# Performance work log

Measured on AMD Instinct MI355X. Metric: run time of the kernel, lower is better.

## Reference

```python
import jax, jax.numpy as jnp
import numpy as np

N, E = 100000, 1600000
N_IN, NHID, HEADS, NOUT = 64, 16, 4, 64
NEG_SLOPE = 0.2


def _p(key, shape, scale=0.1):
    return jax.random.normal(key, shape, dtype=jnp.float32) * scale


def setup_inputs() -> dict:
    key = jax.random.key(0)
    ks = jax.random.split(key, 16)
    H, C1 = HEADS, NHID
    inp = {
        "x": jax.random.normal(ks[0], (N, N_IN), dtype=jnp.float32),
        "edge_index": jax.random.randint(ks[1], (2, E), 0, N, dtype=jnp.int64),
        "frame_mask": jnp.ones((N,), dtype=bool),
        # layer 1: GATv2Conv(N_IN -> NHID, heads=H, concat=True)
        "Wl1": _p(ks[2], (N_IN, H * C1)),
        "bl1": jnp.zeros((H * C1,), jnp.float32),
        "Wr1": _p(ks[3], (N_IN, H * C1)),
        "br1": jnp.zeros((H * C1,), jnp.float32),
        "att1": _p(ks[4], (H, C1)),
        "bo1": jnp.zeros((H * C1,), jnp.float32),
        # layer 2: GATv2Conv(H*NHID -> NOUT, heads=H, concat=False)
        "Wl2": _p(ks[5], (H * C1, H * NOUT)),
        "bl2": jnp.zeros((H * NOUT,), jnp.float32),
        "Wr2": _p(ks[6], (H * C1, H * NOUT)),
        "br2": jnp.zeros((H * NOUT,), jnp.float32),
        "att2": _p(ks[7], (H, NOUT)),
        "bo2": jnp.zeros((NOUT,), jnp.float32),
    }
    return inp


def gatv2_layer(x, src, dst, Wl, bl, Wr, br, att, bo, concat):
    n = x.shape[0]
    H, C = att.shape
    xl = (x @ Wl + bl).reshape(n, H, C)  # source-side transform
    xr = (x @ Wr + br).reshape(n, H, C)  # target-side transform
    # per-edge GATv2 attention: att . leaky_relu(xl[j] + xr[i])
    e = jax.nn.leaky_relu(xl[src] + xr[dst], NEG_SLOPE)  # [E', H, C]
    score = jnp.einsum('ehc,hc->eh', e, att)             # [E', H]
    # scatter-softmax over edges grouped by destination node
    m = jax.ops.segment_max(score, dst, num_segments=n)
    ex = jnp.exp(score - m[dst])
    denom = jax.ops.segment_sum(ex, dst, num_segments=n)
    alpha = ex / (denom[dst] + 1e-16)                    # [E', H]
    out = jax.ops.segment_sum(alpha[:, :, None] * xl[src], dst, num_segments=n)
    out = out.reshape(n, H * C) if concat else out.mean(axis=1)
    return out + bo


def reference(x, edge_index, frame_mask, Wl1, bl1, Wr1, br1, att1, bo1,
              Wl2, bl2, Wr2, br2, att2, bo2):
    n = x.shape[0]
    loops = jnp.arange(n, dtype=edge_index.dtype)
    src = jnp.concatenate([edge_index[0], loops])  # add self-loops (PyG default)
    dst = jnp.concatenate([edge_index[1], loops])
    h = gatv2_layer(x, src, dst, Wl1, bl1, Wr1, br1, att1, bo1, concat=True)
    h = jax.nn.relu(h)
    h = gatv2_layer(h, src, dst, Wl2, bl2, Wr2, br2, att2, bo2, concat=False)
    return jax.nn.relu(h)
```

## Files before the change

kernel.cpp:

```cpp
#include <hip/hip_runtime.h>
#include <hip/hip_bf16.h>
#include <cstdint>
#include <cstddef>

#define NNODES 100000
#define NEDGES 1600000
#define EPLUS  (NEDGES + NNODES)
#define NHEADS 4
#define NB     ((NNODES + 255) / 256)

typedef __hip_bfloat16 bf16;
typedef unsigned short u16;
typedef __attribute__((ext_vector_type(8))) short bf16x8;
typedef __attribute__((ext_vector_type(4))) float f32x4;

#define F_X    0
#define F_WL1  1
#define F_BL1  2
#define F_WR1  3
#define F_BR1  4
#define F_ATT1 5
#define F_BO1  6
#define F_WL2  7
#define F_BL2  8
#define F_WR2  9
#define F_BR2  10
#define F_ATT2 11
#define F_BO2  12
#define F_EI64 13

__device__ __forceinline__ float u2f(u16 s) { return __uint_as_float(((unsigned)s) << 16); }
__device__ __forceinline__ u16  f2u(float f) {
    return __bfloat16_as_ushort(__float2bfloat16(f));
}
__device__ __forceinline__ float ld_any(const void* p, long i, int f32) {
    return f32 ? ((const float*)p)[i] : u2f(((const u16*)p)[i]);
}
__device__ __forceinline__ void cvt_pair(unsigned p, float& lo, float& hi) {
    lo = __uint_as_float(p << 16);
    hi = __uint_as_float(p & 0xffff0000u);
}

__global__ void detect_all(const u16* x, const u16* Wl1, const u16* bl1,
                           const u16* Wr1, const u16* br1, const u16* att1,
                           const u16* bo1, const u16* Wl2, const u16* bl2,
                           const u16* Wr2, const u16* br2, const u16* att2,
                           const u16* bo2, const int* ei, int* flags) {
    const int t = threadIdx.x;
    const u16* ptrs[13] = {x, Wl1, bl1, Wr1, br1, att1, bo1,
                           Wl2, bl2, Wr2, br2, att2, bo2};
    const int cnts[13] = {NNODES * 64, 64 * 64, 64, 64 * 64, 64, 64, 64,
                          64 * 256, 256, 64 * 256, 256, 256, 64};
    if (t < 13) {
        const u16* p = ptrs[t];
        const int cnt = cnts[t];
        int weird = 0, n = 0;
        for (int k = 0; k < 128; ++k) {
            int idx = 2 * k;
            if (idx >= cnt) break;
            u16 v = p[idx];
            n++;
            int ex = (v >> 7) & 0xFF;
            if (v != 0 && (ex < 96 || ex > 143)) weird++;
        }
        flags[t] = (weird * 4 > n) ? 1 : 0;
    } else if (t == 13) {
        int any = 0;
        for (int k = 0; k < 64; ++k) any |= ei[2 * k + 1];
        flags[F_EI64] = (any == 0) ? 1 : 0;
    }
}

__device__ __forceinline__ void edge_sd(const int* __restrict__ ei, int i64,
                                        int e, int& s, int& d) {
    if (e >= NEDGES) { s = d = e - NEDGES; return; }
    if (i64) {
        const long long* p = (const long long*)ei;
        s = (int)p[e]; d = (int)p[NEDGES + e];
    } else {
        s = ei[e]; d = ei[NEDGES + e];
    }
    s = min(max(s, 0), NNODES - 1);
    d = min(max(d, 0), NNODES - 1);
}

#define XB 6250
#define WB 160
#define BB 3
#define HB 6250
__global__ __launch_bounds__(256)
void conv_all(const void* __restrict__ x,
              const void* __restrict__ Wl1, const void* __restrict__ Wr1,
              const void* __restrict__ Wl2, const void* __restrict__ Wr2,
              const void* __restrict__ bl1, const void* __restrict__ br1,
              const void* __restrict__ bl2, const void* __restrict__ br2,
              const int* __restrict__ ei, const int* __restrict__ flags,
              u16* __restrict__ xc, u16* __restrict__ wt1l, u16* __restrict__ wt1r,
              u16* __restrict__ wt2l, u16* __restrict__ wt2r,
              u16* __restrict__ bcs, int* __restrict__ cnt) {
    int b = blockIdx.x;
    if (b < XB) {
        const long i4 = ((long)b * 256 + threadIdx.x) * 4;
        if (i4 < (long)NNODES * 64) {
            if (flags[F_X]) {
                const float4 v = *(const float4*)((const float*)x + i4);
                ushort4 o; o.x=f2u(v.x); o.y=f2u(v.y); o.z=f2u(v.z); o.w=f2u(v.w);
                *(ushort4*)(xc + i4) = o;
            } else {
                *(ushort4*)(xc + i4) = *(const ushort4*)((const u16*)x + i4);
            }
        }
        return;
    }
    b -= XB;
    if (b < WB) {
        const int e = b * 256 + threadIdx.x;
        const void* W; u16* wt; int M, fwi, local;
        if (e < 4096)        { W = Wl1; wt = wt1l; M = 64;  fwi = F_WL1; local = e; }
        else if (e < 8192)   { W = Wr1; wt = wt1r; M = 64;  fwi = F_WR1; local = e - 4096; }
        else if (e < 24576)  { W = Wl2; wt = wt2l; M = 256; fwi = F_WL2; local = e - 8192; }
        else                 { W = Wr2; wt = wt2r; M = 256; fwi = F_WR2; local = e - 24576; }
        const int m = local >> 6, k = local & 63;
        wt[local] = f2u(ld_any(W, (long)k * M + m, flags[fwi]));
        return;
    }
    b -= WB;
    if (b < BB) {
        const int t = b * 256 + threadIdx.x;
        if (t < 64)       bcs[t] = f2u(ld_any(bl1, t,       flags[F_BL1]));
        else if (t < 128) bcs[t] = f2u(ld_any(br1, t - 64,  flags[F_BR1]));
        else if (t < 384) bcs[t] = f2u(ld_any(bl2, t - 128, flags[F_BL2]));
        else if (t < 640) bcs[t] = f2u(ld_any(br2, t - 384, flags[F_BR2]));
        return;
    }
    b -= BB;
    {
        const int e = b * 256 + threadIdx.x;
        if (e >= NEDGES) return;
        int d;
        if (flags[F_EI64]) d = (int)((const long long*)ei)[NEDGES + e];
        else               d = ei[NEDGES + e];
        d = min(max(d, 0), NNODES - 1);
        atomicAdd(&cnt[d], 1);
    }
}

__global__ __launch_bounds__(256)
void scan1_kernel(const int* __restrict__ cnt, int* __restrict__ tmp,
                  int* __restrict__ bsum) {
    __shared__ int sh[256];
    const int idx = blockIdx.x * 256 + threadIdx.x;
    int v = (idx < NNODES) ? cnt[idx] + 1 : 0;
    sh[threadIdx.x] = v;
    __syncthreads();
    for (int off = 1; off < 256; off <<= 1) {
        int t = (threadIdx.x >= off) ? sh[threadIdx.x - off] : 0;
        __syncthreads();
        sh[threadIdx.x] += t;
        __syncthreads();
    }
    if (idx < NNODES) tmp[idx] = sh[threadIdx.x];
    if (threadIdx.x == 255) bsum[blockIdx.x] = sh[255];
}

__global__ __launch_bounds__(512)
void scan2_kernel(int* __restrict__ bsum) {
    __shared__ int sh[512];
    const int t = threadIdx.x;
    sh[t] = (t < NB) ? bsum[t] : 0;
    __syncthreads();
    for (int off = 1; off < 512; off <<= 1) {
        int v = (t >= off) ? sh[t - off] : 0;
        __syncthreads();
        sh[t] += v;
        __syncthreads();
    }
    if (t < NB) bsum[t] = sh[t];
}

__global__ __launch_bounds__(256)
void scan3_kernel(const int* __restrict__ tmp, const int* __restrict__ bsum,
                  int* __restrict__ row_ptr) {
    const int idx = blockIdx.x * 256 + threadIdx.x;
    if (idx < NNODES) {
        int off = (blockIdx.x > 0) ? bsum[blockIdx.x - 1] : 0;
        row_ptr[idx + 1] = tmp[idx] + off;
    }
    if (idx == 0) row_ptr[0] = 0;
}

__global__ __launch_bounds__(256)
void fill_kernel(const int* __restrict__ ei, const int* __restrict__ flags,
                 const int* __restrict__ row_ptr, int* __restrict__ cur,
                 int* __restrict__ csr_src) {
    const int e = blockIdx.x * 256 + threadIdx.x;
    if (e >= EPLUS) return;
    int s, d;
    edge_sd(ei, flags[F_EI64], e, s, d);
    int slot = row_ptr[d] + atomicAdd(&cur[d], 1);
    csr_src[slot] = s;
}

template<int M, int RPB>
__global__ __launch_bounds__(256)
void gemm_mfma(const u16* __restrict__ xc, const u16* __restrict__ wt,
               const u16* __restrict__ bc, u16* __restrict__ out) {
    constexpr int MT = RPB / 16;
    constexpr int NT = M / 64;
    const int wave = threadIdx.x >> 6;
    const int lane = threadIdx.x & 63;
    const int quad = lane >> 4;
    const int l16  = lane & 15;
    const int row0 = blockIdx.x * RPB;
    const int col0 = wave * (M / 4);

    bf16x8 bfrag[NT][2];
#pragma unroll
    for (int nt = 0; nt < NT; ++nt)
#pragma unroll
        for (int c = 0; c < 2; ++c)
            bfrag[nt][c] = *(const bf16x8*)(wt +
                ((size_t)(col0 + nt * 16 + l16) * 64 + c * 32 + quad * 8));

    f32x4 acc[MT][NT];
#pragma unroll
    for (int mt = 0; mt < MT; ++mt)
#pragma unroll
        for (int nt = 0; nt < NT; ++nt)
            acc[mt][nt] = f32x4{0.f, 0.f, 0.f, 0.f};

#pragma unroll
    for (int mt = 0; mt < MT; ++mt) {
        int row = row0 + mt * 16 + l16;
        row = (row < NNODES) ? row : (NNODES - 1);
#pragma unroll
        for (int c = 0; c < 2; ++c) {
            bf16x8 afrag = *(const bf16x8*)(xc + ((size_t)row * 64 + c * 32 + quad * 8));
#pragma unroll
            for (int nt = 0; nt < NT; ++nt)
                acc[mt][nt] = __builtin_amdgcn_mfma_f32_16x16x32_bf16(
                    afrag, bfrag[nt][c], acc[mt][nt], 0, 0, 0);
        }
    }

#pragma unroll
    for (int mt = 0; mt < MT; ++mt) {
#pragma unroll
        for (int nt = 0; nt < NT; ++nt) {
            const int col = col0 + nt * 16 + l16;
            const float bias = u2f(bc[col]);
#pragma unroll
            for (int r = 0; r < 4; ++r) {
                const int row = row0 + mt * 16 + quad * 4 + r;
                if (row < NNODES)
                    out[(size_t)row * M + col] = f2u(acc[mt][nt][r] + bias);
            }
        }
    }
}

template<int HC, bool MEAN, typename TO>
__global__ __launch_bounds__(256)
void fused_gat(const u16* __restrict__ xl, const u16* __restrict__ xr,
               const int* __restrict__ row_ptr, const int* __restrict__ csr_src,
               const void* __restrict__ att, const void* __restrict__ bo,
               const int* __restrict__ flags, int fai, int fbi,
               TO* __restrict__ out) {
    constexpr int VEC = HC / 16;
    constexpr int NU  = VEC / 2;
    const int d = blockIdx.x * 4 + (threadIdx.x >> 6);
    if (d >= NNODES) return;
    const int lane = threadIdx.x & 63;
    const int q = lane >> 4;
    const int l = lane & 15;
    const int fatt = flags[fai];

    float attv[VEC], rv[VEC];
#pragma unroll
    for (int j = 0; j < VEC; ++j)
        attv[j] = ld_any(att, l * VEC + j, fatt);
    {
        const unsigned* rp = (const unsigned*)(xr + (size_t)d * HC + l * VEC);
#pragma unroll
        for (int u = 0; u < NU; ++u) {
            unsigned p = rp[u];
            cvt_pair(p, rv[2 * u], rv[2 * u + 1]);
        }
    }

    const int beg = row_ptr[d], end = row_ptr[d + 1];
    float denom = 1e-16f;
    float acc[VEC];
#pragma unroll
    for (int j = 0; j < VEC; ++j) acc[j] = 0.f;

    unsigned raw[NU];
    {
        int e0 = beg + q;
        int idx = (e0 < end) ? e0 : (end - 1);
        const unsigned* lp = (const unsigned*)(xl + (size_t)csr_src[idx] * HC + l * VEC);
#pragma unroll
        for (int u = 0; u < NU; ++u) raw[u] = lp[u];
    }

    for (int base = beg; base < end; base += 4) {
        float lv[VEC];
#pragma unroll
        for (int u = 0; u < NU; ++u) cvt_pair(raw[u], lv[2 * u], lv[2 * u + 1]);
        if (base + 4 < end) {
            int en = base + 4 + q;
            int idx = (en < end) ? en : (end - 1);
            const unsigned* lp = (const unsigned*)(xl + (size_t)csr_src[idx] * HC + l * VEC);
#pragma unroll
            for (int u = 0; u < NU; ++u) raw[u] = lp[u];
        }
        float part = 0.f;
#pragma unroll
        for (int j = 0; j < VEC; ++j) {
            float v = lv[j] + rv[j];
            v = fmaxf(v, 0.2f * v);
            part = fmaf(v, attv[j], part);
        }
        part += __shfl_xor(part, 1, 64);
        part += __shfl_xor(part, 2, 64);
        float ex = __expf(fminf(part, 60.f));
        ex = (base + q < end) ? ex : 0.f;
        denom += ex;
#pragma unroll
        for (int j = 0; j < VEC; ++j)
            acc[j] = fmaf(ex, lv[j], acc[j]);
    }

    denom += __shfl_xor(denom, 16, 64);
    denom += __shfl_xor(denom, 32, 64);
#pragma unroll
    for (int j = 0; j < VEC; ++j) {
        acc[j] += __shfl_xor(acc[j], 16, 64);
        acc[j] += __shfl_xor(acc[j], 32, 64);
    }
    const float inv = 1.f / denom;

    if constexpr (MEAN) {
#pragma unroll
        for (int j = 0; j < VEC; ++j) {
            acc[j] *= inv;
            acc[j] += __shfl_xor(acc[j], 4, 64);
            acc[j] += __shfl_xor(acc[j], 8, 64);
        }
        if (lane < 4) {
            const int fbo = flags[fbi];
            float* po = (float*)out + (size_t)d * 64 + l * 16;
#pragma unroll
            for (int g = 0; g < 4; ++g) {
                float4 o;
                float* op = (float*)&o;
#pragma unroll
                for (int k = 0; k < 4; ++k) {
                    int c = l * 16 + g * 4 + k;
                    float v = acc[g * 4 + k] * 0.25f + ld_any(bo, c, fbo);
                    op[k] = (v > 0.f) ? v : 0.f;
                }
                *(float4*)(po + g * 4) = o;
            }
        }
    } else {
        if (lane < 16) {
            const int fbo = flags[fbi];
            ushort4 o;
            u16* op = (u16*)&o;
#pragma unroll
            for (int j = 0; j < VEC; ++j) {
                float v = acc[j] * inv + ld_any(bo, l * 4 + j, fbo);
                op[j] = f2u((v > 0.f) ? v : 0.f);
            }
            *(ushort4*)((u16*)out + (size_t)d * 64 + l * 4) = o;
        }
    }
}

__global__ void plant_kernel(float* out, float code) {
    if (code > 0.f) out[0] = code;
}

extern "C" void kernel_launch(void* const* d_in, const int* in_sizes, int n_in,
                              void* d_out, int out_size, void* d_ws, size_t ws_size,
                              hipStream_t stream) {
    int ix = -1, iei = -1;
    int i4096[2], i16384[2], i64s[5], i256[3];
    int c4 = 0, c16 = 0, c64 = 0, c256 = 0;
    bool extra = false;
    for (int i = 0; i < n_in; ++i) {
        int sz = in_sizes[i];
        if (sz == 6400000)      { if (ix < 0) ix = i; else extra = true; }
        else if (sz == 3200000) { if (iei < 0) iei = i; else extra = true; }
        else if (sz == 4096)    { if (c4  < 2) i4096[c4]  = i; c4++;  }
        else if (sz == 16384)   { if (c16 < 2) i16384[c16] = i; c16++; }
        else if (sz == 64)      { if (c64 < 5) i64s[c64]  = i; c64++; }
        else if (sz == 256)     { if (c256 < 3) i256[c256] = i; c256++; }
        else if (sz == 100000 || sz == 1) {  }
        else extra = true;
    }
    bool ok = (ix >= 0) && (iei >= 0) && (c4 == 2) && (c16 == 2)
              && (c64 == 5) && (c256 == 3) && !extra;
    float code = 0.f;
    if (!ok) {
        code = 50000.f + 100.f * (float)n_in;
        ix = 0; iei = 1;
        i4096[0] = 3;  i4096[1] = 5;
        i64s[0] = 4; i64s[1] = 6; i64s[2] = 7; i64s[3] = 8; i64s[4] = 14;
        i16384[0] = 9; i16384[1] = 11;
        i256[0] = 10; i256[1] = 12; i256[2] = 13;
    }

    const u16* x    = (const u16*)d_in[ix];
    const int* ei   = (const int*)d_in[iei];
    const u16* Wl1  = (const u16*)d_in[i4096[0]];
    const u16* Wr1  = (const u16*)d_in[i4096[1]];
    const u16* bl1  = (const u16*)d_in[i64s[0]];
    const u16* br1  = (const u16*)d_in[i64s[1]];
    const u16* att1 = (const u16*)d_in[i64s[2]];
    const u16* bo1  = (const u16*)d_in[i64s[3]];
    const u16* bo2  = (const u16*)d_in[i64s[4]];
    const u16* Wl2  = (const u16*)d_in[i16384[0]];
    const u16* Wr2  = (const u16*)d_in[i16384[1]];
    const u16* bl2  = (const u16*)d_in[i256[0]];
    const u16* br2  = (const u16*)d_in[i256[1]];
    const u16* att2 = (const u16*)d_in[i256[2]];

    char* ws = (char*)d_ws;
    u16* xlb     = (u16*)(ws);
    u16* xrb     = (u16*)(ws + 51200000);
    u16* hbuf    = (u16*)(ws + 102400000);
    u16* xc      = (u16*)(ws + 115200000);
    int* row_ptr = (int*)(ws + 128000000);
    int* cnt     = (int*)(ws + 128400016);
    int* tmp     = (int*)(ws + 128800016);
    int* bsum    = (int*)(ws + 129200016);
    int* csr_src = (int*)(ws + 129201600);
    u16* wt1l    = (u16*)(ws + 136001600);
    u16* wt1r    = (u16*)(ws + 136009792);
    u16* wt2l    = (u16*)(ws + 136017984);
    u16* wt2r    = (u16*)(ws + 136050752);
    u16* bcs     = (u16*)(ws + 136083520);
    int* flags   = (int*)(ws + 136084800);
    const size_t need = 136084864;
    if (ws_size < need) {
        float c2 = 60000.f + (float)(ws_size >> 20);
        code = (c2 > code) ? c2 : code;
    }

    const int node_grid = (NNODES + 3) / 4;
    const int ep_grid   = (EPLUS + 255) / 256;

    detect_all<<<1, 64, 0, stream>>>(x, Wl1, bl1, Wr1, br1, att1, bo1,
                                     Wl2, bl2, Wr2, br2, att2, bo2, ei, flags);

    (void)hipMemsetAsync(cnt, 0, (size_t)NNODES * 4, stream);
    conv_all<<<XB + WB + BB + HB, 256, 0, stream>>>(
        x, Wl1, Wr1, Wl2, Wr2, bl1, br1, bl2, br2, ei, flags,
        xc, wt1l, wt1r, wt2l, wt2r, bcs, cnt);

    scan1_kernel<<<NB, 256, 0, stream>>>(cnt, tmp, bsum);
    scan2_kernel<<<1, 512, 0, stream>>>(bsum);
    scan3_kernel<<<NB, 256, 0, stream>>>(tmp, bsum, row_ptr);
    (void)hipMemsetAsync(cnt, 0, (size_t)NNODES * 4, stream);
    fill_kernel<<<ep_grid, 256, 0, stream>>>(ei, flags, row_ptr, cnt, csr_src);

    gemm_mfma<64, 128><<<(NNODES + 127) / 128, 256, 0, stream>>>(xc, wt1l, bcs,       xlb);
    gemm_mfma<64, 128><<<(NNODES + 127) / 128, 256, 0, stream>>>(xc, wt1r, bcs + 64,  xrb);
    fused_gat<64, false, u16><<<node_grid, 256, 0, stream>>>(
        xlb, xrb, row_ptr, csr_src, att1, bo1, flags, F_ATT1, F_BO1, hbuf);

    gemm_mfma<256, 64><<<(NNODES + 63) / 64, 256, 0, stream>>>(hbuf, wt2l, bcs + 128, xlb);
    gemm_mfma<256, 64><<<(NNODES + 63) / 64, 256, 0, stream>>>(hbuf, wt2r, bcs + 384, xrb);
    fused_gat<256, true, float><<<node_grid, 256, 0, stream>>>(
        xlb, xrb, row_ptr, csr_src, att2, bo2, flags, F_ATT2, F_BO2, (float*)d_out);

    plant_kernel<<<1, 1, 0, stream>>>((float*)d_out, code);
}
```

Measured before the change: 782.0 us.

## Assign one block per node with waves splitting edges and a shared-memory reduction

Restructures the fused GATv2 aggregation kernel so that each destination node gets a full 256-thread block instead of one wave. The four waves take interleaved edges, and each lane owns one or four channels. Partial softmax denominators and accumulators are then combined through shared memory after a barrier. The aim is to improve load balance and per-edge vector width, at the cost of four times as many blocks, a __syncthreads per node, and three waves sitting idle during the final reduction.

```diff
diff --git a/kernel.cpp b/kernel.cpp
--- a/kernel.cpp
+++ b/kernel.cpp
@@ -35,10 +35,6 @@
 }
 __device__ __forceinline__ float ld_any(const void* p, long i, int f32) {
     return f32 ? ((const float*)p)[i] : u2f(((const u16*)p)[i]);
-}
-__device__ __forceinline__ void cvt_pair(unsigned p, float& lo, float& hi) {
-    lo = __uint_as_float(p << 16);
-    hi = __uint_as_float(p & 0xffff0000u);
 }
 
 __global__ void detect_all(const u16* x, const u16* Wl1, const u16* bl1,
@@ -266,53 +262,59 @@
                const void* __restrict__ att, const void* __restrict__ bo,
                const int* __restrict__ flags, int fai, int fbi,
                TO* __restrict__ out) {
-    constexpr int VEC = HC / 16;
-    constexpr int NU  = VEC / 2;
-    const int d = blockIdx.x * 4 + (threadIdx.x >> 6);
-    if (d >= NNODES) return;
+    constexpr int VEC = HC / 64;
+    __shared__ float sh_acc[4][64][VEC];
+    __shared__ float sh_den[4][64];
+    const int d    = blockIdx.x;
+    const int wave = threadIdx.x >> 6;
     const int lane = threadIdx.x & 63;
-    const int q = lane >> 4;
-    const int l = lane & 15;
     const int fatt = flags[fai];
 
     float attv[VEC], rv[VEC];
 #pragma unroll
     for (int j = 0; j < VEC; ++j)
-        attv[j] = ld_any(att, l * VEC + j, fatt);
+        attv[j] = ld_any(att, lane * VEC + j, fatt);
+    if constexpr (VEC == 4) {
+        ushort4 r = *(const ushort4*)(xr + (size_t)d * HC + lane * 4);
+        rv[0]=u2f(r.x); rv[1]=u2f(r.y); rv[2]=u2f(r.z); rv[3]=u2f(r.w);
+    } else {
+        rv[0] = u2f(xr[(size_t)d * HC + lane]);
+    }
+
+    const int beg = row_ptr[d], end = row_ptr[d + 1];
+    float denom = 0.f;
+    float acc[VEC];
+#pragma unroll
+    for (int j = 0; j < VEC; ++j) acc[j] = 0.f;
+
+    int i = beg + wave;
     {
-        const unsigned* rp = (const unsigned*)(xr + (size_t)d * HC + l * VEC);
-#pragma unroll
-        for (int u = 0; u < NU; ++u) {
-            unsigned p = rp[u];
-            cvt_pair(p, rv[2 * u], rv[2 * u + 1]);
-        }
-    }
-
-    const int beg = row_ptr[d], end = row_ptr[d + 1];
-    float denom = 1e-16f;
-    float acc[VEC];
-#pragma unroll
-    for (int j = 0; j < VEC; ++j) acc[j] = 0.f;
-
-    unsigned raw[NU];
+        int idx = (i < end) ? i : (end - 1);
+        (void)idx;
+    }
+    ushort4 a4; u16 a1;
     {
-        int e0 = beg + q;
-        int idx = (e0 < end) ? e0 : (end - 1);
-        const unsigned* lp = (const unsigned*)(xl + (size_t)csr_src[idx] * HC + l * VEC);
-#pragma unroll
-        for (int u = 0; u < NU; ++u) raw[u] = lp[u];
-    }
-
-    for (int base = beg; base < end; base += 4) {
+        int idx = (i < end) ? i : (end - 1);
+        int s0 = csr_src[idx];
+        if constexpr (VEC == 4)
+            a4 = *(const ushort4*)(xl + (size_t)s0 * HC + lane * 4);
+        else
+            a1 = xl[(size_t)s0 * HC + lane];
+    }
+
+    for (; i < end; i += 4) {
         float lv[VEC];
-#pragma unroll
-        for (int u = 0; u < NU; ++u) cvt_pair(raw[u], lv[2 * u], lv[2 * u + 1]);
-        if (base + 4 < end) {
-            int en = base + 4 + q;
-            int idx = (en < end) ? en : (end - 1);
-            const unsigned* lp = (const unsigned*)(xl + (size_t)csr_src[idx] * HC + l * VEC);
-#pragma unroll
-            for (int u = 0; u < NU; ++u) raw[u] = lp[u];
+        if constexpr (VEC == 4) {
+            lv[0]=u2f(a4.x); lv[1]=u2f(a4.y); lv[2]=u2f(a4.z); lv[3]=u2f(a4.w);
+        } else {
+            lv[0] = u2f(a1);
+        }
+        if (i + 4 < end) {
+            int sn = csr_src[i + 4];
+            if constexpr (VEC == 4)
+                a4 = *(const ushort4*)(xl + (size_t)sn * HC + lane * 4);
+            else
+                a1 = xl[(size_t)sn * HC + lane];
         }
         float part = 0.f;
 #pragma unroll
@@ -321,22 +323,31 @@
             v = fmaxf(v, 0.2f * v);
             part = fmaf(v, attv[j], part);
         }
-        part += __shfl_xor(part, 1, 64);
-        part += __shfl_xor(part, 2, 64);
+#pragma unroll
+        for (int off = 8; off >= 1; off >>= 1)
+            part += __shfl_xor(part, off, 64);
         float ex = __expf(fminf(part, 60.f));
-        ex = (base + q < end) ? ex : 0.f;
         denom += ex;
 #pragma unroll
         for (int j = 0; j < VEC; ++j)
             acc[j] = fmaf(ex, lv[j], acc[j]);
     }
 
-    denom += __shfl_xor(denom, 16, 64);
-    denom += __shfl_xor(denom, 32, 64);
+    sh_den[wave][lane] = denom;
+#pragma unroll
+    for (int j = 0; j < VEC; ++j) sh_acc[wave][lane][j] = acc[j];
+    __syncthreads();
+    if (wave != 0) return;
+
+    denom = 1e-16f;
+#pragma unroll
+    for (int w = 0; w < 4; ++w) denom += sh_den[w][lane];
 #pragma unroll
     for (int j = 0; j < VEC; ++j) {
-        acc[j] += __shfl_xor(acc[j], 16, 64);
-        acc[j] += __shfl_xor(acc[j], 32, 64);
+        float a = 0.f;
+#pragma unroll
+        for (int w = 0; w < 4; ++w) a += sh_acc[w][lane][j];
+        acc[j] = a;
     }
     const float inv = 1.f / denom;
 
@@ -344,37 +355,25 @@
 #pragma unroll
         for (int j = 0; j < VEC; ++j) {
             acc[j] *= inv;
-            acc[j] += __shfl_xor(acc[j], 4, 64);
-            acc[j] += __shfl_xor(acc[j], 8, 64);
-        }
-        if (lane < 4) {
-            const int fbo = flags[fbi];
-            float* po = (float*)out + (size_t)d * 64 + l * 16;
-#pragma unroll
-            for (int g = 0; g < 4; ++g) {
-                float4 o;
-                float* op = (float*)&o;
-#pragma unroll
-                for (int k = 0; k < 4; ++k) {
-                    int c = l * 16 + g * 4 + k;
-                    float v = acc[g * 4 + k] * 0.25f + ld_any(bo, c, fbo);
-                    op[k] = (v > 0.f) ? v : 0.f;
-                }
-                *(float4*)(po + g * 4) = o;
-            }
-        }
-    } else {
+            acc[j] += __shfl_xor(acc[j], 16, 64);
+            acc[j] += __shfl_xor(acc[j], 32, 64);
+        }
         if (lane < 16) {
             const int fbo = flags[fbi];
-            ushort4 o;
-            u16* op = (u16*)&o;
+            float4 o;
+            float* op = (float*)&o;
 #pragma unroll
             for (int j = 0; j < VEC; ++j) {
-                float v = acc[j] * inv + ld_any(bo, l * 4 + j, fbo);
-                op[j] = f2u((v > 0.f) ? v : 0.f);
+                float v = acc[j] * 0.25f + ld_any(bo, lane * 4 + j, fbo);
+                op[j] = (v > 0.f) ? v : 0.f;
             }
-            *(ushort4*)((u16*)out + (size_t)d * 64 + l * 4) = o;
-        }
+            *(float4*)((float*)out + (size_t)d * 64 + lane * 4) = o;
+        }
+    } else {
+        const int fbo = flags[fbi];
+        float v = acc[0] * inv + ld_any(bo, lane, fbo);
+        v = (v > 0.f) ? v : 0.f;
+        ((u16*)out)[(size_t)d * 64 + lane] = f2u(v);
     }
 }
 
@@ -449,8 +448,7 @@
         code = (c2 > code) ? c2 : code;
     }
 
-    const int node_grid = (NNODES + 3) / 4;
-    const int ep_grid   = (EPLUS + 255) / 256;
+    const int ep_grid = (EPLUS + 255) / 256;
 
     detect_all<<<1, 64, 0, stream>>>(x, Wl1, bl1, Wr1, br1, att1, bo1,
                                      Wl2, bl2, Wr2, br2, att2, bo2, ei, flags);
@@ -468,12 +466,12 @@
 
     gemm_mfma<64, 128><<<(NNODES + 127) / 128, 256, 0, stream>>>(xc, wt1l, bcs,       xlb);
     gemm_mfma<64, 128><<<(NNODES + 127) / 128, 256, 0, stream>>>(xc, wt1r, bcs + 64,  xrb);
-    fused_gat<64, false, u16><<<node_grid, 256, 0, stream>>>(
+    fused_gat<64, false, u16><<<NNODES, 256, 0, stream>>>(
         xlb, xrb, row_ptr, csr_src, att1, bo1, flags, F_ATT1, F_BO1, hbuf);
 
     gemm_mfma<256, 64><<<(NNODES + 63) / 64, 256, 0, stream>>>(hbuf, wt2l, bcs + 128, xlb);
     gemm_mfma<256, 64><<<(NNODES + 63) / 64, 256, 0, stream>>>(hbuf, wt2r, bcs + 384, xrb);
-    fused_gat<256, true, float><<<node_grid, 256, 0, stream>>>(
+    fused_gat<256, true, float><<<NNODES, 256, 0, stream>>>(
         xlb, xrb, row_ptr, csr_src, att2, bo2, flags, F_ATT2, F_BO2, (float*)d_out);
 
     plant_kernel<<<1, 1, 0, stream>>>((float*)d_out, code);
```

Measured after the change: 805.2 us. 1.03x slower.

## Merge left/right GEMMs into one launch and remap layer-2 GAT to one edge per wave

Applied to the files above, without the earlier changes.

The left and right projection GEMMs for each layer now run as a single launch, with blockIdx.y choosing the weight, bias and output set. This removes two launches and lets the two halves run concurrently. The layer-2 attention kernel now processes one edge per wave iteration, with all 64 lanes covering the 256 channels at 4 each and a two-deep prefetch of gathered rows. Before, each quarter-wave handled a separate edge with 16 values per lane. The new mapping uses fewer registers and gives wider coalesced gathers, but needs more iterations and a longer shuffle reduction per edge.

```diff
diff --git a/kernel.cpp b/kernel.cpp
--- a/kernel.cpp
+++ b/kernel.cpp
@@ -35,10 +35,6 @@
 }
 __device__ __forceinline__ float ld_any(const void* p, long i, int f32) {
     return f32 ? ((const float*)p)[i] : u2f(((const u16*)p)[i]);
-}
-__device__ __forceinline__ void cvt_pair(unsigned p, float& lo, float& hi) {
-    lo = __uint_as_float(p << 16);
-    hi = __uint_as_float(p & 0xffff0000u);
 }
 
 __global__ void detect_all(const u16* x, const u16* Wl1, const u16* bl1,
@@ -203,10 +199,15 @@
 
 template<int M, int RPB>
 __global__ __launch_bounds__(256)
-void gemm_mfma(const u16* __restrict__ xc, const u16* __restrict__ wt,
-               const u16* __restrict__ bc, u16* __restrict__ out) {
+void gemm_mfma(const u16* __restrict__ xc,
+               const u16* __restrict__ wtl, const u16* __restrict__ wtr,
+               const u16* __restrict__ bcl, const u16* __restrict__ bcr,
+               u16* __restrict__ outl, u16* __restrict__ outr) {
     constexpr int MT = RPB / 16;
     constexpr int NT = M / 64;
+    const u16* wt = blockIdx.y ? wtr : wtl;
+    const u16* bc = blockIdx.y ? bcr : bcl;
+    u16* out      = blockIdx.y ? outr : outl;
     const int wave = threadIdx.x >> 6;
     const int lane = threadIdx.x & 63;
     const int quad = lane >> 4;
@@ -259,64 +260,49 @@
     }
 }
 
-template<int HC, bool MEAN, typename TO>
-__global__ __launch_bounds__(256)
-void fused_gat(const u16* __restrict__ xl, const u16* __restrict__ xr,
-               const int* __restrict__ row_ptr, const int* __restrict__ csr_src,
-               const void* __restrict__ att, const void* __restrict__ bo,
-               const int* __restrict__ flags, int fai, int fbi,
-               TO* __restrict__ out) {
-    constexpr int VEC = HC / 16;
-    constexpr int NU  = VEC / 2;
+__global__ __launch_bounds__(256)
+void gat_l1(const u16* __restrict__ xl, const u16* __restrict__ xr,
+            const int* __restrict__ row_ptr, const int* __restrict__ csr_src,
+            const void* __restrict__ att, const void* __restrict__ bo,
+            const int* __restrict__ flags, u16* __restrict__ out) {
     const int d = blockIdx.x * 4 + (threadIdx.x >> 6);
     if (d >= NNODES) return;
     const int lane = threadIdx.x & 63;
     const int q = lane >> 4;
     const int l = lane & 15;
-    const int fatt = flags[fai];
-
-    float attv[VEC], rv[VEC];
-#pragma unroll
-    for (int j = 0; j < VEC; ++j)
-        attv[j] = ld_any(att, l * VEC + j, fatt);
+    const int fatt = flags[F_ATT1];
+
+    float attv[4], rv[4];
+#pragma unroll
+    for (int j = 0; j < 4; ++j)
+        attv[j] = ld_any(att, l * 4 + j, fatt);
     {
-        const unsigned* rp = (const unsigned*)(xr + (size_t)d * HC + l * VEC);
-#pragma unroll
-        for (int u = 0; u < NU; ++u) {
-            unsigned p = rp[u];
-            cvt_pair(p, rv[2 * u], rv[2 * u + 1]);
-        }
+        ushort4 r = *(const ushort4*)(xr + (size_t)d * 64 + l * 4);
+        rv[0]=u2f(r.x); rv[1]=u2f(r.y); rv[2]=u2f(r.z); rv[3]=u2f(r.w);
     }
 
     const int beg = row_ptr[d], end = row_ptr[d + 1];
     float denom = 1e-16f;
-    float acc[VEC];
-#pragma unroll
-    for (int j = 0; j < VEC; ++j) acc[j] = 0.f;
-
-    unsigned raw[NU];
+    float acc[4] = {0.f, 0.f, 0.f, 0.f};
+
+    ushort4 a4;
     {
         int e0 = beg + q;
         int idx = (e0 < end) ? e0 : (end - 1);
-        const unsigned* lp = (const unsigned*)(xl + (size_t)csr_src[idx] * HC + l * VEC);
-#pragma unroll
-        for (int u = 0; u < NU; ++u) raw[u] = lp[u];
+        a4 = *(const ushort4*)(xl + (size_t)csr_src[idx] * 64 + l * 4);
     }
 
     for (int base = beg; base < end; base += 4) {
-        float lv[VEC];
-#pragma unroll
-        for (int u = 0; u < NU; ++u) cvt_pair(raw[u], lv[2 * u], lv[2 * u + 1]);
+        float lv[4];
+        lv[0]=u2f(a4.x); lv[1]=u2f(a4.y); lv[2]=u2f(a4.z); lv[3]=u2f(a4.w);
         if (base + 4 < end) {
             int en = base + 4 + q;
             int idx = (en < end) ? en : (end - 1);
-            const unsigned* lp = (const unsigned*)(xl + (size_t)csr_src[idx] * HC + l * VEC);
-#pragma unroll
-            for (int u = 0; u < NU; ++u) raw[u] = lp[u];
+            a4 = *(const ushort4*)(xl + (size_t)csr_src[idx] * 64 + l * 4);
         }
         float part = 0.f;
 #pragma unroll
-        for (int j = 0; j < VEC; ++j) {
+        for (int j = 0; j < 4; ++j) {
             float v = lv[j] + rv[j];
             v = fmaxf(v, 0.2f * v);
             part = fmaf(v, attv[j], part);
@@ -327,54 +313,122 @@
         ex = (base + q < end) ? ex : 0.f;
         denom += ex;
 #pragma unroll
-        for (int j = 0; j < VEC; ++j)
+        for (int j = 0; j < 4; ++j)
             acc[j] = fmaf(ex, lv[j], acc[j]);
     }
 
     denom += __shfl_xor(denom, 16, 64);
     denom += __shfl_xor(denom, 32, 64);
 #pragma unroll
-    for (int j = 0; j < VEC; ++j) {
+    for (int j = 0; j < 4; ++j) {
         acc[j] += __shfl_xor(acc[j], 16, 64);
         acc[j] += __shfl_xor(acc[j], 32, 64);
     }
     const float inv = 1.f / denom;
 
-    if constexpr (MEAN) {
-#pragma unroll
-        for (int j = 0; j < VEC; ++j) {
-            acc[j] *= inv;
-            acc[j] += __shfl_xor(acc[j], 4, 64);
-            acc[j] += __shfl_xor(acc[j], 8, 64);
-        }
-        if (lane < 4) {
-            const int fbo = flags[fbi];
-            float* po = (float*)out + (size_t)d * 64 + l * 16;
-#pragma unroll
-            for (int g = 0; g < 4; ++g) {
-                float4 o;
-                float* op = (float*)&o;
-#pragma unroll
-                for (int k = 0; k < 4; ++k) {
-                    int c = l * 16 + g * 4 + k;
-                    float v = acc[g * 4 + k] * 0.25f + ld_any(bo, c, fbo);
-                    op[k] = (v > 0.f) ? v : 0.f;
-                }
-                *(float4*)(po + g * 4) = o;
+    if (lane < 16) {
+        const int fbo = flags[F_BO1];
+        ushort4 o;
+        u16* op = (u16*)&o;
+#pragma unroll
+        for (int j = 0; j < 4; ++j) {
+            float v = acc[j] * inv + ld_any(bo, l * 4 + j, fbo);
+            op[j] = f2u((v > 0.f) ? v : 0.f);
+        }
+        *(ushort4*)(out + (size_t)d * 64 + l * 4) = o;
+    }
+}
+
+__global__ __launch_bounds__(256)
+void gat_l2(const u16* __restrict__ xl, const u16* __restrict__ xr,
+            const int* __restrict__ row_ptr, const int* __restrict__ csr_src,
+            const void* __restrict__ att, const void* __restrict__ bo,
+            const int* __restrict__ flags, float* __restrict__ out) {
+    const int d = blockIdx.x * 4 + (threadIdx.x >> 6);
+    if (d >= NNODES) return;
+    const int lane = threadIdx.x & 63;
+    const int fatt = flags[F_ATT2];
+
+    float attv[4], rv[4];
+#pragma unroll
+    for (int j = 0; j < 4; ++j)
+        attv[j] = ld_any(att, lane * 4 + j, fatt);
+    {
+        ushort4 r = *(const ushort4*)(xr + (size_t)d * 256 + lane * 4);
+        rv[0]=u2f(r.x); rv[1]=u2f(r.y); rv[2]=u2f(r.z); rv[3]=u2f(r.w);
+    }
+
+    const int beg = row_ptr[d], end = row_ptr[d + 1];
+    float denom = 1e-16f;
+    float acc[4] = {0.f, 0.f, 0.f, 0.f};
+
+    ushort4 b0, b1;
+    b0 = *(const ushort4*)(xl + (size_t)csr_src[beg] * 256 + lane * 4);
+    if (beg + 1 < end)
+        b1 = *(const ushort4*)(xl + (size_t)csr_src[beg + 1] * 256 + lane * 4);
+
+    for (int i = beg; i < end; i += 2) {
+        {
+            float lv[4];
+            lv[0]=u2f(b0.x); lv[1]=u2f(b0.y); lv[2]=u2f(b0.z); lv[3]=u2f(b0.w);
+            if (i + 2 < end)
+                b0 = *(const ushort4*)(xl + (size_t)csr_src[i + 2] * 256 + lane * 4);
+            float part = 0.f;
+#pragma unroll
+            for (int j = 0; j < 4; ++j) {
+                float v = lv[j] + rv[j];
+                v = fmaxf(v, 0.2f * v);
+                part = fmaf(v, attv[j], part);
             }
-        }
-    } else {
-        if (lane < 16) {
-            const int fbo = flags[fbi];
-            ushort4 o;
-            u16* op = (u16*)&o;
-#pragma unroll
-            for (int j = 0; j < VEC; ++j) {
-                float v = acc[j] * inv + ld_any(bo, l * 4 + j, fbo);
-                op[j] = f2u((v > 0.f) ? v : 0.f);
+#pragma unroll
+            for (int off = 8; off >= 1; off >>= 1)
+                part += __shfl_xor(part, off, 64);
+            float ex = __expf(fminf(part, 60.f));
+            denom += ex;
+#pragma unroll
+            for (int j = 0; j < 4; ++j)
+                acc[j] = fmaf(ex, lv[j], acc[j]);
+        }
+        if (i + 1 < end) {
+            float lv[4];
+            lv[0]=u2f(b1.x); lv[1]=u2f(b1.y); lv[2]=u2f(b1.z); lv[3]=u2f(b1.w);
+            if (i + 3 < end)
+                b1 = *(const ushort4*)(xl + (size_t)csr_src[i + 3] * 256 + lane * 4);
+            float part = 0.f;
+#pragma unroll
+            for (int j = 0; j < 4; ++j) {
+                float v = lv[j] + rv[j];
+                v = fmaxf(v, 0.2f * v);
+                part = fmaf(v, attv[j], part);
             }
-            *(ushort4*)((u16*)out + (size_t)d * 64 + l * 4) = o;
-        }
+#pragma unroll
+            for (int off = 8; off >= 1; off >>= 1)
+                part += __shfl_xor(part, off, 64);
+            float ex = __expf(fminf(part, 60.f));
+            denom += ex;
+#pragma unroll
+            for (int j = 0; j < 4; ++j)
+                acc[j] = fmaf(ex, lv[j], acc[j]);
+        }
+    }
+
+    const float inv = 1.f / denom;
+#pragma unroll
+    for (int j = 0; j < 4; ++j) {
+        acc[j] *= inv;
+        acc[j] += __shfl_xor(acc[j], 16, 64);
+        acc[j] += __shfl_xor(acc[j], 32, 64);
+    }
+    if (lane < 16) {
+        const int fbo = flags[F_BO2];
+        float4 o;
+        float* op = (float*)&o;
+#pragma unroll
+        for (int j = 0; j < 4; ++j) {
+            float v = acc[j] * 0.25f + ld_any(bo, lane * 4 + j, fbo);
+            op[j] = (v > 0.f) ? v : 0.f;
+        }
+        *(float4*)(out + (size_t)d * 64 + lane * 4) = o;
     }
 }
 
@@ -466,15 +520,15 @@
     (void)hipMemsetAsync(cnt, 0, (size_t)NNODES * 4, stream);
     fill_kernel<<<ep_grid, 256, 0, stream>>>(ei, flags, row_ptr, cnt, csr_src);
 
-    gemm_mfma<64, 128><<<(NNODES + 127) / 128, 256, 0, stream>>>(xc, wt1l, bcs,       xlb);
-    gemm_mfma<64, 128><<<(NNODES + 127) / 128, 256, 0, stream>>>(xc, wt1r, bcs + 64,  xrb);
-    fused_gat<64, false, u16><<<node_grid, 256, 0, stream>>>(
-        xlb, xrb, row_ptr, csr_src, att1, bo1, flags, F_ATT1, F_BO1, hbuf);
-
-    gemm_mfma<256, 64><<<(NNODES + 63) / 64, 256, 0, stream>>>(hbuf, wt2l, bcs + 128, xlb);
-    gemm_mfma<256, 64><<<(NNODES + 63) / 64, 256, 0, stream>>>(hbuf, wt2r, bcs + 384, xrb);
-    fused_gat<256, true, float><<<node_grid, 256, 0, stream>>>(
-        xlb, xrb, row_ptr, csr_src, att2, bo2, flags, F_ATT2, F_BO2, (float*)d_out);
+    gemm_mfma<64, 128><<<dim3((NNODES + 127) / 128, 2), 256, 0, stream>>>(
+        xc, wt1l, wt1r, bcs, bcs + 64, xlb, xrb);
+    gat_l1<<<node_grid, 256, 0, stream>>>(
+        xlb, xrb, row_ptr, csr_src, att1, bo1, flags, hbuf);
+
+    gemm_mfma<256, 64><<<dim3((NNODES + 63) / 64, 2), 256, 0, stream>>>(
+        hbuf, wt2l, wt2r, bcs + 128, bcs + 384, xlb, xrb);
+    gat_l2<<<node_grid, 256, 0, stream>>>(
+        xlb, xrb, row_ptr, csr_src, att2, bo2, flags, (float*)d_out);
 
     plant_kernel<<<1, 1, 0, stream>>>((float*)d_out, code);
 }
```

After: 667.9 us. -14.6%, faster.
